# Performance work log

Measured on AMD Instinct MI355X. Metric: run time of the kernel, lower is better.

Reference implementation:

```python
import math
import jax, jax.numpy as jnp
import numpy as np

ALPHA = 0.7

def setup_inputs() -> dict:
    key = jax.random.key(0)
    ks = jax.random.split(key, 4)
    T, V, Q, F, D = 256, 256, 32, 64, 512
    return {
        "text_embed": jax.random.normal(ks[0], (T, D), dtype=jnp.float32),
        "clip_embed": jax.random.normal(ks[1], (V, D), dtype=jnp.float32),
        "concept_embeds": jax.random.normal(ks[2], (T, Q, D), dtype=jnp.float32),
        "frame_embeds": jax.random.normal(ks[3], (V, F, D), dtype=jnp.float32),
        "logit_scale": jnp.array(math.log(1.0 / 0.07), dtype=jnp.float32),
    }

def _l2norm(x, eps=1e-12):
    # matches F.normalize(dim=-1): x / max(||x||, eps)
    n = jnp.sqrt(jnp.sum(x * x, axis=-1, keepdims=True))
    return x / jnp.maximum(n, eps)

def reference(text_embed, clip_embed, concept_embeds, frame_embeds, logit_scale):
    scale = jnp.minimum(jnp.exp(logit_scale), 100.0)
    # global similarity: [T, V]
    g_sim = scale * (text_embed @ clip_embed.T)
    # local MaxSim: normalize, dot products, max over frames f, mean over tokens q
    nc = _l2norm(concept_embeds.astype(jnp.float32))  # [T, Q, D]
    nf = _l2norm(frame_embeds.astype(jnp.float32))    # [V, F, D]
    scores = jnp.einsum('tqd,vfd->tvqf', nc, nf)      # [T, V, Q, F]
    max_scores = jnp.max(scores, axis=-1)             # [T, V, Q]
    l_sim = scale * jnp.mean(max_scores, axis=-1)     # [T, V]
    return ALPHA * g_sim + (1.0 - ALPHA) * l_sim
```

## Files before the change

kernel.cpp:

```cpp
#include <hip/hip_runtime.h>
#include <stdint.h>

#define ALPHA_ 0.7f
constexpr int Tn = 256, Vn = 256, Qn = 32, Fn = 64, Dn = 512;
constexpr int Mn = Tn * Qn;
constexpr int Nn = Vn * Fn;
constexpr int Kn = Dn;
constexpr int NOT = 8;
constexpr int GT  = (Kn / 64) * NOT;

typedef float  f32x4  __attribute__((ext_vector_type(4)));
typedef __bf16 bf16x8 __attribute__((ext_vector_type(8)));

static __device__ __forceinline__ unsigned short f2bf(float f) {
  uint32_t x = __builtin_bit_cast(uint32_t, f);
  x += 0x7fffu + ((x >> 16) & 1u);
  return (unsigned short)(x >> 16);
}

static __device__ __forceinline__ void gload_lds16(const void* g, void* l) {
  __builtin_amdgcn_global_load_lds(
      (const __attribute__((address_space(1))) uint32_t*)g,
      (__attribute__((address_space(3))) uint32_t*)l, 16, 0, 0);
}

#define BAR()   asm volatile("s_barrier" ::: "memory")
#define LGKM0() do { asm volatile("s_waitcnt lgkmcnt(0)" ::: "memory"); \
                     __builtin_amdgcn_sched_barrier(0); } while (0)
#define VM6()   asm volatile("s_waitcnt vmcnt(6)" ::: "memory")
#define VM0()   asm volatile("s_waitcnt vmcnt(0)" ::: "memory")

__global__ void normalize_rows(const float* __restrict__ src,
                               uint4* __restrict__ dst) {
  const int wave = threadIdx.x >> 6;
  const int lane = threadIdx.x & 63;
  const int row  = blockIdx.x * 4 + wave;
  const float4* p = reinterpret_cast<const float4*>(src + (size_t)row * Dn + lane * 8);
  float4 x0 = p[0];
  float4 x1 = p[1];
  float ss = x0.x*x0.x + x0.y*x0.y + x0.z*x0.z + x0.w*x0.w
           + x1.x*x1.x + x1.y*x1.y + x1.z*x1.z + x1.w*x1.w;
  #pragma unroll
  for (int m = 1; m < 64; m <<= 1) ss += __shfl_xor(ss, m, 64);
  const float inv = 1.0f / fmaxf(sqrtf(ss), 1e-12f);
  union { unsigned short u[8]; uint4 v; } pk;
  const float f[8] = {x0.x, x0.y, x0.z, x0.w, x1.x, x1.y, x1.z, x1.w};
  #pragma unroll
  for (int j = 0; j < 8; ++j) pk.u[j] = f2bf(f[j] * inv);
  dst[(size_t)row * (Dn / 8) + lane] = pk.v;
}

__global__ __launch_bounds__(512, 2)
void maxsim256_kernel(const uint16_t* __restrict__ Abf,
                      const uint16_t* __restrict__ Bbf,
                      const float* __restrict__ text,
                      const float* __restrict__ clip,
                      const float* __restrict__ logit_scale,
                      float* __restrict__ out) {
  __shared__ __align__(16) unsigned char lds[131072];
  const int tid  = threadIdx.x;
  const int lane = tid & 63;
  const int wave = tid >> 6;
  const int wr   = wave >> 2;
  const int wc   = wave & 3;
  const int bid  = blockIdx.x;
  const int nx0  = (bid & 7) * 8;
  const int by   = bid >> 3;

  const float scale = fminf(expf(logit_scale[0]), 100.0f);
  const float coefG = ALPHA_ * scale;
  const float coefL = (1.0f - ALPHA_) * scale * (1.0f / (float)Qn);

  const char* Ag  = reinterpret_cast<const char*>(Abf) + (size_t)by  * 262144;
  const char* Bg0 = reinterpret_cast<const char*>(Bbf) + (size_t)nx0 * 262144;

  unsigned srcA[2], srcB[2], ldsoff[2];
  #pragma unroll
  for (int j = 0; j < 2; ++j) {
    const unsigned r = (j * 8 + wave) * 8 + (lane >> 3);
    const unsigned c = (((lane & 7) ^ (lane >> 3)) << 4);
    srcA[j]  = (((r >> 6) << 7) + (r & 63)) * 1024 + c;
    srcB[j]  = (((r >> 5) << 6) + (r & 31)) * 1024 + c;
    ldsoff[j] = (j * 8 + wave) * 1024;
  }

  auto stage = [&](int buf, int isB, int h, int g) {
    const unsigned base = buf * 65536 + isB * 32768 + h * 16384;
    const unsigned kt = (g & 7) * 128;
    #pragma unroll
    for (int j = 0; j < 2; ++j) {
      const void* src = isB
          ? (const void*)(Bg0 + (size_t)((g >> 3) * 262144 + h * 32768 + kt + srcB[j]))
          : (const void*)(Ag  + (size_t)(h * 65536 + kt + srcA[j]));
      gload_lds16(src, &lds[base + ldsoff[j]]);
    }
  };

  f32x4 acc[8][4];
  #pragma unroll
  for (int i = 0; i < 8; ++i)
    #pragma unroll
    for (int j = 0; j < 4; ++j)
      acc[i][j] = {0.f, 0.f, 0.f, 0.f};

  bf16x8 af[4][2];
  bf16x8 bq[4][2];

  const int rA  = lane & 15;
  const int kg  = lane >> 4;
  const unsigned key = (unsigned)(rA & 7) << 4;

  auto ldA = [&](int buf, int h) {
    const unsigned b = buf * 65536 + h * 16384;
    #pragma unroll
    for (int m = 0; m < 4; ++m) {
      const unsigned s = (unsigned)(wr * 64 + m * 16 + rA);
      #pragma unroll
      for (int kk = 0; kk < 2; ++kk) {
        const unsigned kb = kk * 64 + kg * 16;
        af[m][kk] = *reinterpret_cast<const bf16x8*>(&lds[b + s * 128 + (kb ^ key)]);
      }
    }
  };
  auto ldB = [&](int buf, int h) {
    const unsigned b = buf * 65536 + 32768 + h * 16384;
    #pragma unroll
    for (int n = 0; n < 2; ++n) {
      const unsigned s = (unsigned)(wc * 32 + n * 16 + rA);
      #pragma unroll
      for (int kk = 0; kk < 2; ++kk) {
        const unsigned kb = kk * 64 + kg * 16;
        bq[h * 2 + n][kk] = *reinterpret_cast<const bf16x8*>(&lds[b + s * 128 + (kb ^ key)]);
      }
    }
  };
  auto mfma_quad = [&](int hm, int hn) {
    __builtin_amdgcn_s_setprio(1);
    #pragma unroll
    for (int m = 0; m < 4; ++m)
      #pragma unroll
      for (int n = 0; n < 2; ++n)
        #pragma unroll
        for (int kk = 0; kk < 2; ++kk) {
          const int mi = hm * 4 + m, ni = hn * 2 + n;
          acc[mi][ni] = __builtin_amdgcn_mfma_f32_16x16x32_bf16(
              af[m][kk], bq[ni][kk], acc[mi][ni], 0, 0, 0);
        }
    __builtin_amdgcn_s_setprio(0);
  };

  auto epilogue = [&](int ot) {
    const int v_out = (nx0 + ot) * 4 + wc;
    const float4* cp = reinterpret_cast<const float4*>(clip + (size_t)v_out * Dn) + lane * 2;
    const float4 c0 = cp[0], c1 = cp[1];
    float4 t0[4], t1[4];
    #pragma unroll
    for (int gq = 0; gq < 4; ++gq) {
      const float4* tp = reinterpret_cast<const float4*>(
          text + (size_t)(by * 8 + wr * 4 + gq) * Dn) + lane * 2;
      t0[gq] = tp[0]; t1[gq] = tp[1];
    }
    #pragma unroll
    for (int gq = 0; gq < 4; ++gq) {
      float sum = 0.f;
      #pragma unroll
      for (int m2 = 0; m2 < 2; ++m2) {
        const int mi = gq * 2 + m2;
        #pragma unroll
        for (int reg = 0; reg < 4; ++reg) {
          float rm = fmaxf(fmaxf(acc[mi][0][reg], acc[mi][1][reg]),
                           fmaxf(acc[mi][2][reg], acc[mi][3][reg]));
          rm = fmaxf(rm, __shfl_xor(rm, 1, 64));
          rm = fmaxf(rm, __shfl_xor(rm, 2, 64));
          rm = fmaxf(rm, __shfl_xor(rm, 4, 64));
          rm = fmaxf(rm, __shfl_xor(rm, 8, 64));
          sum += rm;
        }
      }
      sum += __shfl_xor(sum, 16, 64);
      sum += __shfl_xor(sum, 32, 64);
      float gd = t0[gq].x*c0.x + t0[gq].y*c0.y + t0[gq].z*c0.z + t0[gq].w*c0.w
               + t1[gq].x*c1.x + t1[gq].y*c1.y + t1[gq].z*c1.z + t1[gq].w*c1.w;
      gd += __shfl_xor(gd, 1, 64);  gd += __shfl_xor(gd, 2, 64);
      gd += __shfl_xor(gd, 4, 64);  gd += __shfl_xor(gd, 8, 64);
      gd += __shfl_xor(gd, 16, 64); gd += __shfl_xor(gd, 32, 64);
      if (lane == 0)
        out[(by * 8 + wr * 4 + gq) * Vn + v_out] = coefG * gd + coefL * sum;
    }
    #pragma unroll
    for (int i = 0; i < 8; ++i)
      #pragma unroll
      for (int j = 0; j < 4; ++j)
        acc[i][j] = {0.f, 0.f, 0.f, 0.f};
  };

  stage(0, 0, 0, 0); stage(0, 1, 0, 0); stage(0, 1, 1, 0); stage(0, 0, 1, 0);
  stage(1, 0, 0, 1); stage(1, 1, 0, 1); stage(1, 1, 1, 1);
  VM6(); BAR();

  auto tile_step = [&](int g, int buf) {
    ldA(buf, 0); ldB(buf, 0);
    if (g + 1 < GT) stage(buf ^ 1, 0, 1, g + 1);
    asm volatile("s_waitcnt lgkmcnt(8)" ::: "memory");
    BAR(); LGKM0();
    mfma_quad(0, 0);
    BAR();
    ldB(buf, 1);
    if (g + 2 < GT) stage(buf, 0, 0, g + 2);
    BAR(); LGKM0();
    mfma_quad(0, 1);
    BAR();
    ldA(buf, 1);
    if (g + 2 < GT) stage(buf, 1, 0, g + 2);
    BAR(); LGKM0();
    mfma_quad(1, 1);
    BAR();
    if (g + 2 < GT) stage(buf, 1, 1, g + 2);
    BAR();
    mfma_quad(1, 0);
    if (g < GT - 2) { VM6(); } else { VM0(); }
    if ((g & 7) == 7) epilogue(g >> 3);
    BAR();
  };

  for (int t = 0; t < GT; t += 2) {
    tile_step(t, 0);
    tile_step(t + 1, 1);
  }
}

extern "C" void kernel_launch(void* const* d_in, const int* in_sizes, int n_in,
                              void* d_out, int out_size, void* d_ws, size_t ws_size,
                              hipStream_t stream) {
  const float* text        = (const float*)d_in[0];
  const float* clip        = (const float*)d_in[1];
  const float* concept     = (const float*)d_in[2];
  const float* frames      = (const float*)d_in[3];
  const float* logit_scale = (const float*)d_in[4];
  float* out = (float*)d_out;

  uint16_t* Abf = (uint16_t*)d_ws;
  uint16_t* Bbf = Abf + (size_t)Mn * Kn;

  normalize_rows<<<Mn / 4, 256, 0, stream>>>(concept, (uint4*)Abf);
  normalize_rows<<<Nn / 4, 256, 0, stream>>>(frames, (uint4*)Bbf);
  maxsim256_kernel<<<256, 512, 0, stream>>>(Abf, Bbf, text, clip, logit_scale, out);
}
```

Baseline: 228.6 us.

## Restructure MFMA tile step to cut barriers and batch LDS reads and stages

The per-tile schedule now issues the A-half-0 and both B-half LDS fragment reads up front. It uses partial lgkmcnt waits so the first MFMA half can start while the remaining reads land. The three next-tile global-to-LDS stages are grouped after one barrier, which cuts the barriers per tile step from about seven to two. The epilogue also loads text rows one at a time instead of holding all four in registers, to ease register pressure. The risk is weaker interleaving of memory traffic with MFMA work, and subtler reliance on waitcnt ordering for buffer-reuse safety.

```diff
diff --git a/kernel.cpp b/kernel.cpp
--- a/kernel.cpp
+++ b/kernel.cpp
@@ -25,8 +25,9 @@
 }
 
 #define BAR()   asm volatile("s_barrier" ::: "memory")
-#define LGKM0() do { asm volatile("s_waitcnt lgkmcnt(0)" ::: "memory"); \
-                     __builtin_amdgcn_sched_barrier(0); } while (0)
+#define SBAR()  __builtin_amdgcn_sched_barrier(0)
+#define LGKM(N) do { asm volatile("s_waitcnt lgkmcnt(" #N ")" ::: "memory"); \
+                     SBAR(); } while (0)
 #define VM6()   asm volatile("s_waitcnt vmcnt(6)" ::: "memory")
 #define VM0()   asm volatile("s_waitcnt vmcnt(0)" ::: "memory")
 
@@ -134,8 +135,7 @@
       }
     }
   };
-  auto mfma_quad = [&](int hm, int hn) {
-    __builtin_amdgcn_s_setprio(1);
+  auto mfma_half = [&](int hm, int hn) {
     #pragma unroll
     for (int m = 0; m < 4; ++m)
       #pragma unroll
@@ -146,20 +146,12 @@
           acc[mi][ni] = __builtin_amdgcn_mfma_f32_16x16x32_bf16(
               af[m][kk], bq[ni][kk], acc[mi][ni], 0, 0, 0);
         }
-    __builtin_amdgcn_s_setprio(0);
   };
 
   auto epilogue = [&](int ot) {
     const int v_out = (nx0 + ot) * 4 + wc;
     const float4* cp = reinterpret_cast<const float4*>(clip + (size_t)v_out * Dn) + lane * 2;
     const float4 c0 = cp[0], c1 = cp[1];
-    float4 t0[4], t1[4];
-    #pragma unroll
-    for (int gq = 0; gq < 4; ++gq) {
-      const float4* tp = reinterpret_cast<const float4*>(
-          text + (size_t)(by * 8 + wr * 4 + gq) * Dn) + lane * 2;
-      t0[gq] = tp[0]; t1[gq] = tp[1];
-    }
     #pragma unroll
     for (int gq = 0; gq < 4; ++gq) {
       float sum = 0.f;
@@ -179,8 +171,11 @@
       }
       sum += __shfl_xor(sum, 16, 64);
       sum += __shfl_xor(sum, 32, 64);
-      float gd = t0[gq].x*c0.x + t0[gq].y*c0.y + t0[gq].z*c0.z + t0[gq].w*c0.w
-               + t1[gq].x*c1.x + t1[gq].y*c1.y + t1[gq].z*c1.z + t1[gq].w*c1.w;
+      const float4* tp = reinterpret_cast<const float4*>(
+          text + (size_t)(by * 8 + wr * 4 + gq) * Dn) + lane * 2;
+      const float4 t0 = tp[0], t1 = tp[1];
+      float gd = t0.x*c0.x + t0.y*c0.y + t0.z*c0.z + t0.w*c0.w
+               + t1.x*c1.x + t1.y*c1.y + t1.z*c1.z + t1.w*c1.w;
       gd += __shfl_xor(gd, 1, 64);  gd += __shfl_xor(gd, 2, 64);
       gd += __shfl_xor(gd, 4, 64);  gd += __shfl_xor(gd, 8, 64);
       gd += __shfl_xor(gd, 16, 64); gd += __shfl_xor(gd, 32, 64);
@@ -200,24 +195,31 @@
 
   auto tile_step = [&](int g, int buf) {
     ldA(buf, 0); ldB(buf, 0);
+    SBAR();
+    ldB(buf, 1);
+    SBAR();
     if (g + 1 < GT) stage(buf ^ 1, 0, 1, g + 1);
-    asm volatile("s_waitcnt lgkmcnt(8)" ::: "memory");
-    BAR(); LGKM0();
-    mfma_quad(0, 0);
-    BAR();
-    ldB(buf, 1);
-    if (g + 2 < GT) stage(buf, 0, 0, g + 2);
-    BAR(); LGKM0();
-    mfma_quad(0, 1);
+    LGKM(4);
+    __builtin_amdgcn_s_setprio(1);
+    mfma_half(0, 0);
+    __builtin_amdgcn_s_setprio(0);
+    LGKM(0);
+    __builtin_amdgcn_s_setprio(1);
+    mfma_half(0, 1);
+    __builtin_amdgcn_s_setprio(0);
     BAR();
     ldA(buf, 1);
-    if (g + 2 < GT) stage(buf, 1, 0, g + 2);
-    BAR(); LGKM0();
-    mfma_quad(1, 1);
-    BAR();
-    if (g + 2 < GT) stage(buf, 1, 1, g + 2);
-    BAR();
-    mfma_quad(1, 0);
+    SBAR();
+    if (g + 2 < GT) {
+      stage(buf, 0, 0, g + 2);
+      stage(buf, 1, 0, g + 2);
+      stage(buf, 1, 1, g + 2);
+    }
+    LGKM(0);
+    __builtin_amdgcn_s_setprio(1);
+    mfma_half(1, 1);
+    mfma_half(1, 0);
+    __builtin_amdgcn_s_setprio(0);
     if (g < GT - 2) { VM6(); } else { VM0(); }
     if ((g & 7) == 7) epilogue(g >> 3);
     BAR();
```

Result: faster. 221.2 us (-3.3%).
